# Performance work log

Measured on AMD Instinct MI355X. Metric: run time of the kernel, lower is better.

Reference implementation:

```python
import jax, jax.numpy as jnp
import numpy as np
from jax import lax

H = 512; VS = 32000; VT = 32000; B = 64; TS = 64; TT = 51
PAD = 0


def _lstm_dir(xt, Wih, Whh, bih, bhh):
    # xt: (T, b, h); PyTorch LSTM gate order i,f,g,o
    b = xt.shape[1]
    h0 = jnp.zeros((b, Wih.shape[0] // 4), xt.dtype)
    def step(carry, x):
        h, c = carry
        g = x @ Wih.T + bih + h @ Whh.T + bhh
        i, f, gg, o = jnp.split(g, 4, axis=1)
        c = jax.nn.sigmoid(f) * c + jax.nn.sigmoid(i) * jnp.tanh(gg)
        h = jax.nn.sigmoid(o) * jnp.tanh(c)
        return (h, c), h
    (hT, cT), hs = lax.scan(step, (h0, h0), xt)
    return hs, hT, cT


def _forward(source, target, emb_src, emb_tgt, enc_Wih_f, enc_Whh_f, enc_bih_f, enc_bhh_f,
             enc_Wih_b, enc_Whh_b, enc_bih_b, enc_bhh_b, Wh_w, Wh_b,
             dec_Wih, dec_Whh, dec_bih, dec_bhh, Ws_w, Ws_b, v_w, v_b,
             lin_w, lin_b, out_w, out_b):
    b, ts = source.shape
    h = emb_src.shape[1]
    es = emb_src.at[PAD].set(0.0)  # padding_idx=0 (also zeroes its grad)
    et = emb_tgt.at[PAD].set(0.0)
    # ---- Encoder: bidirectional LSTM, directions summed (all lengths equal) ----
    x = es[source]                       # (b, ts, h); dropout skipped (eval)
    xt = jnp.swapaxes(x, 0, 1)           # (ts, b, h)
    hs_f, hT_f, cT_f = _lstm_dir(xt, enc_Wih_f, enc_Whh_f, enc_bih_f, enc_bhh_f)
    hs_b, hT_b, cT_b = _lstm_dir(xt[::-1], enc_Wih_b, enc_Whh_b, enc_bih_b, enc_bhh_b)
    hs_b = hs_b[::-1]
    enc_out = jnp.swapaxes(hs_f + hs_b, 0, 1)   # (b, ts, h)
    hx = hT_f + hT_b                             # (b, h)
    cx = cT_f + cT_b
    enc_feat_bth = (enc_out.reshape(-1, h) @ Wh_w.T + Wh_b).reshape(b, ts, h)
    # Faithful quirk: mask is eq(PAD) (padding positions = 1), and (ts,b)->(b,ts) is a raw reshape
    mask_bT = (source.T == PAD).astype(x.dtype).reshape(b, ts)
    tgt = target.T  # (tt, b)

    def step(carry, inp):
        hx, cx = carry
        wf, wt = inp
        e = et[wf]                                        # (b, h)
        g = e @ dec_Wih.T + dec_bih + hx @ dec_Whh.T + dec_bhh
        i, f, gg, o = jnp.split(g, 4, axis=1)
        cx = jax.nn.sigmoid(f) * cx + jax.nn.sigmoid(i) * jnp.tanh(gg)
        hx = jax.nn.sigmoid(o) * jnp.tanh(cx)
        # Bahdanau attention
        dec_f = hx @ Ws_w.T + Ws_b
        att = jnp.tanh(enc_feat_bth + dec_f[:, None, :])  # (b, ts, h)
        scores = att @ v_w[0] + v_b[0]                    # (b, ts)
        attn = jax.nn.softmax(scores, axis=1) * mask_bT
        # Faithful quirk: torch .view(-1, b, n) on contiguous (b, ts, n) = raw reshape
        a = attn.reshape(ts, b, 1)
        eo = enc_out.reshape(ts, b, h)
        content = jnp.sum(a * eo, axis=0)                 # (b, h)
        hx_new = jnp.tanh(jnp.concatenate([content, hx], axis=1) @ lin_w.T + lin_b)
        logits = hx_new @ out_w.T + out_b                 # (b, VT)
        logp = jax.nn.log_softmax(logits, axis=1)
        ce = -jnp.take_along_axis(logp, wt[:, None], axis=1)[:, 0]
        valid = (wt != PAD).astype(logits.dtype)          # ignore_index=0
        cnt = valid.sum()
        step_loss = jnp.where(cnt > 0, (ce * valid).sum() / jnp.maximum(cnt, 1.0), 0.0)
        return (hx, cx), step_loss

    (_, _), losses = lax.scan(step, (hx, cx), (tgt[:-1], tgt[1:]))
    return losses.sum()


def setup_inputs() -> dict:
    key = jax.random.key(0)
    ks = jax.random.split(key, 30)
    p = lambda i, s: 0.02 * jax.random.normal(ks[i], s, dtype=jnp.float32)
    return {
        "source": jax.random.randint(ks[0], (B, TS), 0, VS),
        "target": jax.random.randint(ks[1], (B, TT), 0, VT),
        "emb_src": p(2, (VS, H)), "emb_tgt": p(3, (VT, H)),
        "enc_Wih_f": p(4, (4 * H, H)), "enc_Whh_f": p(5, (4 * H, H)),
        "enc_bih_f": p(6, (4 * H,)), "enc_bhh_f": p(7, (4 * H,)),
        "enc_Wih_b": p(8, (4 * H, H)), "enc_Whh_b": p(9, (4 * H, H)),
        "enc_bih_b": p(10, (4 * H,)), "enc_bhh_b": p(11, (4 * H,)),
        "Wh_w": p(12, (H, H)), "Wh_b": p(13, (H,)),
        "dec_Wih": p(14, (4 * H, H)), "dec_Whh": p(15, (4 * H, H)),
        "dec_bih": p(16, (4 * H,)), "dec_bhh": p(17, (4 * H,)),
        "Ws_w": p(18, (H, H)), "Ws_b": p(19, (H,)),
        "v_w": p(20, (1, H)), "v_b": p(21, (1,)),
        "lin_w": p(22, (H, 2 * H)), "lin_b": p(23, (H,)),
        "out_w": p(24, (VT, H)), "out_b": p(25, (VT,)),
    }


def reference(source, target, emb_src, emb_tgt, enc_Wih_f, enc_Whh_f, enc_bih_f, enc_bhh_f,
              enc_Wih_b, enc_Whh_b, enc_bih_b, enc_bhh_b, Wh_w, Wh_b,
              dec_Wih, dec_Whh, dec_bih, dec_bhh, Ws_w, Ws_b, v_w, v_b,
              lin_w, lin_b, out_w, out_b):
    return _forward(source, target, emb_src, emb_tgt, enc_Wih_f, enc_Whh_f, enc_bih_f, enc_bhh_f,
                    enc_Wih_b, enc_Whh_b, enc_bih_b, enc_bhh_b, Wh_w, Wh_b,
                    dec_Wih, dec_Whh, dec_bih, dec_bhh, Ws_w, Ws_b, v_w, v_b,
                    lin_w, lin_b, out_w, out_b)
```

## Files before the change

kernel.cpp:

```cpp
#include <hip/hip_runtime.h>


#define DI __device__ __forceinline__

typedef __attribute__((ext_vector_type(8))) short bf16x8;
typedef __attribute__((ext_vector_type(4))) short s16x4;
typedef __attribute__((ext_vector_type(4))) float f32x4;
typedef const __attribute__((address_space(1))) void* gp1_t;
typedef __attribute__((address_space(3))) void* lp3_t;

DI float bf2f(short u) {
    union { float f; unsigned u; } c; c.u = ((unsigned)(unsigned short)u) << 16; return c.f;
}
DI short f2bf(float f) {
    union { float f; unsigned u; } c; c.f = f;
    unsigned r = c.u + 0x7fffu + ((c.u >> 16) & 1u);
    return (short)(r >> 16);
}
DI float sigm(float x) { return 1.f / (1.f + __expf(-x)); }
DI float tanh_(float x) {
    float e = __expf(-2.f * fabsf(x));
    float r = (1.f - e) / (1.f + e);
    return copysignf(r, x);
}

template<int EPI>
__global__ __launch_bounds__(256) void gemm128(
    const short* __restrict__ A, int lda,
    const short* __restrict__ B, int ldb,
    int K,
    const float* __restrict__ bias,
    void* __restrict__ Cout, int ldc,
    float* __restrict__ partial, int pstride)
{
    __shared__ short lA[8192], lB[8192];
    const int tid = threadIdx.x;
    const int lane = tid & 63, wave = tid >> 6;
    const int wr = wave >> 1, wc = wave & 1;
    const int mbase = blockIdx.y * 128, nbase = blockIdx.x * 128;

    const char* ga[4]; const char* gb[4];
    {
        int r = tid >> 3, sl = tid & 7;
#pragma unroll
        for (int R = 0; R < 4; ++R) {
            int row = R * 32 + r;
            int so = (sl ^ (row & 7)) << 4;
            ga[R] = (const char*)(A + (size_t)(mbase + row) * lda) + so;
            gb[R] = (const char*)(B + (size_t)(nbase + row) * ldb) + so;
        }
    }
    const int r7 = lane & 7, gq = lane >> 4;
    int abase[4], bbase[4];
#pragma unroll
    for (int i = 0; i < 4; ++i) {
        abase[i] = (wr * 64 + i * 16 + (lane & 15)) * 128;
        bbase[i] = (wc * 64 + i * 16 + (lane & 15)) * 128;
    }
    int sloff[2];
#pragma unroll
    for (int h = 0; h < 2; ++h) sloff[h] = ((h * 4 + gq) ^ r7) << 4;

    f32x4 acc[4][4];
#pragma unroll
    for (int i = 0; i < 4; ++i)
#pragma unroll
        for (int j = 0; j < 4; ++j) acc[i][j] = (f32x4){0.f, 0.f, 0.f, 0.f};

    for (int kk = 0; kk < K; kk += 64) {
#pragma unroll
        for (int R = 0; R < 4; ++R)
            __builtin_amdgcn_global_load_lds((gp1_t)ga[R],
                (lp3_t)((char*)lA + R * 4096 + tid * 16), 16, 0, 0);
#pragma unroll
        for (int R = 0; R < 4; ++R)
            __builtin_amdgcn_global_load_lds((gp1_t)gb[R],
                (lp3_t)((char*)lB + R * 4096 + tid * 16), 16, 0, 0);
#pragma unroll
        for (int R = 0; R < 4; ++R) { ga[R] += 128; gb[R] += 128; }
        __syncthreads();
#pragma unroll
        for (int h = 0; h < 2; ++h) {
            bf16x8 af[4], bfv[4];
#pragma unroll
            for (int i = 0; i < 4; ++i)
                af[i] = *(const bf16x8*)((const char*)lA + abase[i] + sloff[h]);
#pragma unroll
            for (int j = 0; j < 4; ++j)
                bfv[j] = *(const bf16x8*)((const char*)lB + bbase[j] + sloff[h]);
#pragma unroll
            for (int i = 0; i < 4; ++i)
#pragma unroll
                for (int j = 0; j < 4; ++j)
                    acc[i][j] = __builtin_amdgcn_mfma_f32_16x16x32_bf16(
                        af[i], bfv[j], acc[i][j], 0, 0, 0);
        }
        __syncthreads();
    }

    float bv[4];
#pragma unroll
    for (int j = 0; j < 4; ++j) bv[j] = bias[nbase + wc * 64 + j * 16 + (lane & 15)];

    if constexpr (EPI == 3) {
#pragma unroll
        for (int i = 0; i < 4; ++i)
#pragma unroll
            for (int r = 0; r < 4; ++r) {
                float es = 0.f;
#pragma unroll
                for (int j = 0; j < 4; ++j) es += __expf(acc[i][j][r] + bv[j]);
                es += __shfl_xor(es, 1); es += __shfl_xor(es, 2);
                es += __shfl_xor(es, 4); es += __shfl_xor(es, 8);
                if ((lane & 15) == 0) {
                    int row = mbase + wr * 64 + i * 16 + (lane >> 4) * 4 + r;
                    partial[(size_t)row * pstride + blockIdx.x * 2 + wc] = es;
                }
            }
    } else {
#pragma unroll
        for (int i = 0; i < 4; ++i)
#pragma unroll
            for (int j = 0; j < 4; ++j)
#pragma unroll
                for (int r = 0; r < 4; ++r) {
                    int row = mbase + wr * 64 + i * 16 + (lane >> 4) * 4 + r;
                    int col = nbase + wc * 64 + j * 16 + (lane & 15);
                    float v = acc[i][j][r] + bv[j];
                    if constexpr (EPI == 0)
                        ((float*)Cout)[(size_t)row * ldc + col] = v;
                    else if constexpr (EPI == 1)
                        ((short*)Cout)[(size_t)row * ldc + col] = f2bf(tanh_(v));
                    else
                        ((short*)Cout)[(size_t)row * ldc + col] = f2bf(v);
                }
    }
}

DI void gbar(int* bar, int target)
{
    __syncthreads();
    if (threadIdx.x == 0) {
        __threadfence();
        atomicAdd(bar, 1);
        while (__hip_atomic_load(bar, __ATOMIC_RELAXED, __HIP_MEMORY_SCOPE_AGENT) < target)
            __builtin_amdgcn_s_sleep(2);
        __threadfence();
    }
    __syncthreads();
}

struct EncDir {
    const short* Whh;
    const short* pre;
    short* hslots;
    float* hs;
    float* cfin;
};

__global__ __launch_bounds__(256) void enc_kernel(EncDir F, EncDir Bd, int* bar)
{
    const int isB = (blockIdx.x >= 32) ? 1 : 0;
    const EncDir E = isB ? Bd : F;
    const int nb = blockIdx.x & 31;
    const int tid = threadIdx.x, lane = tid & 63, wave = tid >> 6;
    const int lc = wave * 16 + (lane & 15);
    const int ncol = nb * 64 + lc;

    bf16x8 bq[16];
    {
        const short* bp = E.Whh + (size_t)ncol * 512 + ((lane >> 4) * 8);
#pragma unroll
        for (int ks = 0; ks < 16; ++ks) bq[ks] = *(const bf16x8*)(bp + ks * 32);
    }
    float cr[4] = {0.f, 0.f, 0.f, 0.f};

    __shared__ short hl[32768];
    __shared__ float g[64 * 65];

    const int swave = tid >> 6, ssl = tid & 63;
    const int r7 = lane & 7, gq = lane >> 4;
    const int hb_base = (lane & 15) << 10;

    for (int s = 0; s < 64; ++s) {
        const char* hsrc = (const char*)E.hslots + (size_t)s * 65536;
#pragma unroll
        for (int R = 0; R < 16; ++R) {
            int row = R * 4 + swave;
            __builtin_amdgcn_global_load_lds(
                (gp1_t)(hsrc + row * 1024 + ((ssl ^ (row & 7)) << 4)),
                (lp3_t)((char*)hl + R * 4096 + tid * 16), 16, 0, 0);
        }
        __syncthreads();

        f32x4 acc[4];
#pragma unroll
        for (int i = 0; i < 4; ++i) acc[i] = (f32x4){0.f, 0.f, 0.f, 0.f};
#pragma unroll
        for (int ks = 0; ks < 16; ++ks) {
            const char* hb = (const char*)hl + hb_base + (((ks * 4 + gq) ^ r7) << 4);
#pragma unroll
            for (int mt = 0; mt < 4; ++mt)
                acc[mt] = __builtin_amdgcn_mfma_f32_16x16x32_bf16(
                    *(const bf16x8*)(hb + mt * 16384), bq[ks], acc[mt], 0, 0, 0);
        }
#pragma unroll
        for (int mt = 0; mt < 4; ++mt)
#pragma unroll
            for (int r = 0; r < 4; ++r)
                g[(mt * 16 + gq * 4 + r) * 65 + lc] = acc[mt][r];
        __syncthreads();

        const int tf = isB ? (63 - s) : s;
        const short* prr = E.pre + (size_t)tf * 131072;
        short* hw = E.hslots + (size_t)(s + 1) * 32768;
        float* hsw = E.hs + (size_t)tf * 32768;
#pragma unroll
        for (int it = 0; it < 4; ++it) {
            int item = tid + it * 256, b = item >> 4, jj = item & 15;
            int j = nb * 16 + jj;
            s16x4 pv = *(const s16x4*)(prr + b * 2048 + nb * 64 + jj * 4);
            float gi = g[b * 65 + jj * 4 + 0] + bf2f(pv.x);
            float gf = g[b * 65 + jj * 4 + 1] + bf2f(pv.y);
            float gg = g[b * 65 + jj * 4 + 2] + bf2f(pv.z);
            float go = g[b * 65 + jj * 4 + 3] + bf2f(pv.w);
            float cn = sigm(gf) * cr[it] + sigm(gi) * tanh_(gg);
            float h = sigm(go) * tanh_(cn);
            cr[it] = cn;
            hw[b * 512 + j] = f2bf(h);
            hsw[b * 512 + j] = h;
            if (s == 63) E.cfin[b * 512 + j] = cn;
        }
        gbar(bar, 64 * (s + 1));
    }
}

__global__ __launch_bounds__(256) void dec_kernel(
    const short* __restrict__ Whh, const short* __restrict__ pre,
    short* __restrict__ hslots, const float* __restrict__ c0,
    short* __restrict__ cat, int* __restrict__ bar)
{
    const int nb = blockIdx.x;
    const int tid = threadIdx.x, lane = tid & 63, wave = tid >> 6;
    const int lc = wave * 16 + (lane & 15);
    const int ncol = nb * 64 + lc;

    bf16x8 bq[16];
    {
        const short* bp = Whh + (size_t)ncol * 512 + ((lane >> 4) * 8);
#pragma unroll
        for (int ks = 0; ks < 16; ++ks) bq[ks] = *(const bf16x8*)(bp + ks * 32);
    }
    float cr[4];
#pragma unroll
    for (int it = 0; it < 4; ++it) {
        int item = tid + it * 256, b = item >> 4, jj = item & 15;
        cr[it] = c0[b * 512 + nb * 16 + jj];
    }

    __shared__ short hl[32768];
    __shared__ float g[64 * 65];
    const int swave = tid >> 6, ssl = tid & 63;
    const int r7 = lane & 7, gq = lane >> 4;
    const int hb_base = (lane & 15) << 10;

    for (int t = 0; t < 50; ++t) {
        const char* hsrc = (const char*)hslots + (size_t)t * 65536;
#pragma unroll
        for (int R = 0; R < 16; ++R) {
            int row = R * 4 + swave;
            __builtin_amdgcn_global_load_lds(
                (gp1_t)(hsrc + row * 1024 + ((ssl ^ (row & 7)) << 4)),
                (lp3_t)((char*)hl + R * 4096 + tid * 16), 16, 0, 0);
        }
        __syncthreads();

        f32x4 acc[4];
#pragma unroll
        for (int i = 0; i < 4; ++i) acc[i] = (f32x4){0.f, 0.f, 0.f, 0.f};
#pragma unroll
        for (int ks = 0; ks < 16; ++ks) {
            const char* hb = (const char*)hl + hb_base + (((ks * 4 + gq) ^ r7) << 4);
#pragma unroll
            for (int mt = 0; mt < 4; ++mt)
                acc[mt] = __builtin_amdgcn_mfma_f32_16x16x32_bf16(
                    *(const bf16x8*)(hb + mt * 16384), bq[ks], acc[mt], 0, 0, 0);
        }
#pragma unroll
        for (int mt = 0; mt < 4; ++mt)
#pragma unroll
            for (int r = 0; r < 4; ++r)
                g[(mt * 16 + gq * 4 + r) * 65 + lc] = acc[mt][r];
        __syncthreads();

        const short* prr = pre + (size_t)t * 131072;
        short* hw = hslots + (size_t)(t + 1) * 32768;
        short* cw = cat + (size_t)t * 65536 + 512;
#pragma unroll
        for (int it = 0; it < 4; ++it) {
            int item = tid + it * 256, b = item >> 4, jj = item & 15;
            int j = nb * 16 + jj;
            s16x4 pv = *(const s16x4*)(prr + b * 2048 + nb * 64 + jj * 4);
            float gi = g[b * 65 + jj * 4 + 0] + bf2f(pv.x);
            float gf = g[b * 65 + jj * 4 + 1] + bf2f(pv.y);
            float gg = g[b * 65 + jj * 4 + 2] + bf2f(pv.z);
            float go = g[b * 65 + jj * 4 + 3] + bf2f(pv.w);
            float cn = sigm(gf) * cr[it] + sigm(gi) * tanh_(gg);
            float h = sigm(go) * tanh_(cn);
            cr[it] = cn;
            hw[b * 512 + j] = f2bf(h);
            cw[b * 1024 + j] = f2bf(h);
        }
        gbar(bar, 32 * (t + 1));
    }
}

struct PrepArgs {
    const float *Wih_f, *Whh_f, *Wih_b, *Whh_b, *Wih_d, *Whh_d;
    short *oWih_f, *oWhh_f, *oWih_b, *oWhh_b, *oWih_d, *oWhh_d;
    const float *Ws, *Wh, *lin, *outw;
    short *oWs, *oWh, *olin, *oout;
    const float *emb_src, *emb_tgt;
    const int *source, *target;
    short *A_src, *A_tgt;
    const float *bihf, *bhhf, *bihb, *bhhb, *bihd, *bhhd;
    float *bsumf, *bsumb, *bsumd;
    int *tgtf;
    short *hF0, *hB0;
    float *dout;
    int *bar;
};

__global__ __launch_bounds__(256) void prep_kernel(PrepArgs P)
{
    const long long total = 6291456LL + 262144 + 262144 + 524288 + 16384000
                          + 2097152 + 1638400 + 6144 + 3200 + 65536 + 3;
    for (long long i = (long long)blockIdx.x * 256 + threadIdx.x; i < total;
         i += (long long)gridDim.x * 256) {
        long long t = i;
        if (t < 6291456LL) {
            int seg = (int)(t >> 20); int r = (int)(t & 1048575);
            int n = r >> 9, k = r & 511;
            int orig = (n & 3) * 512 + (n >> 2);
            const float* s; short* d;
            switch (seg) {
                case 0: s = P.Wih_f; d = P.oWih_f; break;
                case 1: s = P.Whh_f; d = P.oWhh_f; break;
                case 2: s = P.Wih_b; d = P.oWih_b; break;
                case 3: s = P.Whh_b; d = P.oWhh_b; break;
                case 4: s = P.Wih_d; d = P.oWih_d; break;
                default: s = P.Whh_d; d = P.oWhh_d; break;
            }
            d[n * 512 + k] = f2bf(s[orig * 512 + k]);
            continue;
        }
        t -= 6291456LL;
        if (t < 262144) { P.oWs[t] = f2bf(P.Ws[t]); continue; } t -= 262144;
        if (t < 262144) { P.oWh[t] = f2bf(P.Wh[t]); continue; } t -= 262144;
        if (t < 524288) { P.olin[t] = f2bf(P.lin[t]); continue; } t -= 524288;
        if (t < 16384000) { P.oout[t] = f2bf(P.outw[t]); continue; } t -= 16384000;
        if (t < 2097152) {
            int r = (int)(t >> 9), k = (int)(t & 511);
            int tt = r >> 6, b = r & 63;
            int tok = P.source[b * 64 + tt];
            P.A_src[t] = tok ? f2bf(P.emb_src[(size_t)tok * 512 + k]) : (short)0;
            continue;
        } t -= 2097152;
        if (t < 1638400) {
            int r = (int)(t >> 9), k = (int)(t & 511);
            int tt = r >> 6, b = r & 63;
            int tok = P.target[b * 51 + tt];
            P.A_tgt[t] = tok ? f2bf(P.emb_tgt[(size_t)tok * 512 + k]) : (short)0;
            continue;
        } t -= 1638400;
        if (t < 6144) {
            int net = (int)(t >> 11); int n = (int)(t & 2047);
            int orig = (n & 3) * 512 + (n >> 2);
            if (net == 0)      P.bsumf[n] = P.bihf[orig] + P.bhhf[orig];
            else if (net == 1) P.bsumb[n] = P.bihb[orig] + P.bhhb[orig];
            else               P.bsumd[n] = P.bihd[orig] + P.bhhd[orig];
            continue;
        } t -= 6144;
        if (t < 3200) {
            int s = (int)t >> 6, b = (int)t & 63;
            P.tgtf[t] = P.target[b * 51 + s + 1];
            continue;
        } t -= 3200;
        if (t < 65536) {
            if (t < 32768) P.hF0[t] = 0; else P.hB0[t - 32768] = 0;
            continue;
        } t -= 65536;
        if (t == 0) P.dout[0] = 0.f;
        else P.bar[t - 1] = 0;
    }
}

__global__ __launch_bounds__(256) void mid_kernel(
    const float* __restrict__ hsF, const float* __restrict__ hsB,
    const float* __restrict__ cFf, const float* __restrict__ cBf,
    float* __restrict__ enc_out, short* __restrict__ enc_out_bf,
    short* __restrict__ hx0, float* __restrict__ cdec0)
{
    const int total = 64 * 64 * 512 + 64 * 512;
    for (int i = blockIdx.x * 256 + threadIdx.x; i < total; i += gridDim.x * 256) {
        if (i < 64 * 64 * 512) {
            int r = i >> 9, d = i & 511;
            int b = r >> 6, tt = r & 63;
            float v = hsF[(size_t)(tt * 64 + b) * 512 + d] + hsB[(size_t)(tt * 64 + b) * 512 + d];
            enc_out[i] = v;
            enc_out_bf[i] = f2bf(v);
        } else {
            int j = i - 64 * 64 * 512;
            int b = j >> 9, d = j & 511;
            float h0 = hsF[(size_t)(63 * 64 + b) * 512 + d] + hsB[(size_t)(0 * 64 + b) * 512 + d];
            hx0[b * 512 + d] = f2bf(h0);
            cdec0[b * 512 + d] = cFf[b * 512 + d] + cBf[b * 512 + d];
        }
    }
}

__global__ __launch_bounds__(256) void attn_scores(
    const float* __restrict__ enc_feat, const float* __restrict__ dec_f,
    const float* __restrict__ v_w, const float* __restrict__ v_b,
    float* __restrict__ scores)
{
    int p = blockIdx.y;
    int tp = blockIdx.x * 64 + p;
    __shared__ float df[512], vw[512];
    for (int i = threadIdx.x; i < 512; i += 256) {
        df[i] = dec_f[(size_t)tp * 512 + i];
        vw[i] = v_w[i];
    }
    __syncthreads();
    int lane = threadIdx.x & 63, wave = threadIdx.x >> 6;
    float vb = v_b[0];
    for (int q = wave; q < 64; q += 4) {
        const float* ef = enc_feat + (size_t)(p * 64 + q) * 512;
        float s = 0.f;
        for (int d = lane; d < 512; d += 64)
            s += tanh_(ef[d] + df[d]) * vw[d];
        for (int o = 32; o > 0; o >>= 1) s += __shfl_xor(s, o);
        if (lane == 0) scores[(size_t)tp * 64 + q] = s + vb;
    }
}

__global__ __launch_bounds__(256) void softmax_mask(
    float* __restrict__ attn, const int* __restrict__ source)
{
    int row = blockIdx.x * 4 + (threadIdx.x >> 6);
    int lane = threadIdx.x & 63;
    int p = row & 63;
    float v = attn[(size_t)row * 64 + lane];
    float m = v;
    for (int o = 32; o > 0; o >>= 1) m = fmaxf(m, __shfl_xor(m, o));
    float e = __expf(v - m);
    float s = e;
    for (int o = 32; o > 0; o >>= 1) s += __shfl_xor(s, o);
    float mask = (source[lane * 64 + p] == 0) ? 1.f : 0.f;
    attn[(size_t)row * 64 + lane] = (e / s) * mask;
}

__global__ __launch_bounds__(256) void content_cat(
    const float* __restrict__ attn, const float* __restrict__ enc_out,
    short* __restrict__ cat)
{
    int q = blockIdx.y;
    int tq = blockIdx.x * 64 + q;
    __shared__ float ac[64];
    if (threadIdx.x < 64)
        ac[threadIdx.x] = attn[(size_t)(blockIdx.x * 64 + threadIdx.x) * 64 + q];
    __syncthreads();
    for (int d = threadIdx.x; d < 512; d += 256) {
        float s = 0.f;
#pragma unroll 8
        for (int pp = 0; pp < 64; ++pp)
            s += ac[pp] * enc_out[(size_t)(pp * 64 + q) * 512 + d];
        cat[(size_t)tq * 1024 + d] = f2bf(s);
    }
}

__global__ __launch_bounds__(256) void loss_kernel(
    const float* __restrict__ partial, const short* __restrict__ hxnew,
    const short* __restrict__ outw, const float* __restrict__ outb,
    const int* __restrict__ tgtf, float* __restrict__ out)
{
    int t = blockIdx.x;
    int tid = threadIdx.x;
    int b = tid >> 2, c = tid & 3;
    int row = t * 64 + b;
    float s = 0.f;
    for (int j = c; j < 500; j += 4) s += partial[(size_t)row * 500 + j];
    int w = tgtf[row];
    const short* hp = hxnew + (size_t)row * 512 + c * 128;
    const short* wp = outw + (size_t)w * 512 + c * 128;
    float tl = 0.f;
    for (int k2 = 0; k2 < 128; k2 += 8) {
        bf16x8 hv = *(const bf16x8*)(hp + k2);
        bf16x8 wv = *(const bf16x8*)(wp + k2);
#pragma unroll
        for (int u = 0; u < 8; ++u) tl += bf2f(hv[u]) * bf2f(wv[u]);
    }
    s += __shfl_xor(s, 1); s += __shfl_xor(s, 2);
    tl += __shfl_xor(tl, 1); tl += __shfl_xor(tl, 2);
    __shared__ float ce_s[64], va_s[64];
    if (c == 0) {
        float lse = logf(s);
        float ce = lse - (tl + outb[w]);
        float valid = (w != 0) ? 1.f : 0.f;
        ce_s[b] = ce * valid;
        va_s[b] = valid;
    }
    __syncthreads();
    if (tid < 64) {
        float cv = ce_s[tid], vv = va_s[tid];
        for (int o = 32; o > 0; o >>= 1) { cv += __shfl_xor(cv, o); vv += __shfl_xor(vv, o); }
        if (tid == 0) {
            float sl = (vv > 0.f) ? cv / fmaxf(vv, 1.f) : 0.f;
            atomicAdd(out, sl);
        }
    }
}

extern "C" void kernel_launch(void* const* d_in, const int* in_sizes, int n_in,
                              void* d_out, int out_size, void* d_ws, size_t ws_size,
                              hipStream_t stream)
{
    (void)in_sizes; (void)n_in; (void)out_size; (void)ws_size;
    const int*   source  = (const int*)  d_in[0];
    const int*   target  = (const int*)  d_in[1];
    const float* emb_src = (const float*)d_in[2];
    const float* emb_tgt = (const float*)d_in[3];
    const float* eWihF   = (const float*)d_in[4];
    const float* eWhhF   = (const float*)d_in[5];
    const float* ebihF   = (const float*)d_in[6];
    const float* ebhhF   = (const float*)d_in[7];
    const float* eWihB   = (const float*)d_in[8];
    const float* eWhhB   = (const float*)d_in[9];
    const float* ebihB   = (const float*)d_in[10];
    const float* ebhhB   = (const float*)d_in[11];
    const float* Wh_w    = (const float*)d_in[12];
    const float* Wh_b    = (const float*)d_in[13];
    const float* dWih    = (const float*)d_in[14];
    const float* dWhh    = (const float*)d_in[15];
    const float* dbih    = (const float*)d_in[16];
    const float* dbhh    = (const float*)d_in[17];
    const float* Ws_w    = (const float*)d_in[18];
    const float* Ws_b    = (const float*)d_in[19];
    const float* v_w     = (const float*)d_in[20];
    const float* v_b     = (const float*)d_in[21];
    const float* lin_w   = (const float*)d_in[22];
    const float* lin_b   = (const float*)d_in[23];
    const float* out_w   = (const float*)d_in[24];
    const float* out_b   = (const float*)d_in[25];

    char* base = (char*)d_ws;
    size_t off = 0;
    auto alloc = [&](size_t bytes) -> char* {
        char* p = base + off;
        off = (off + bytes + 255) & ~(size_t)255;
        return p;
    };
    short* WihF_bf = (short*)alloc(1048576ULL * 2);
    short* WhhF_bf = (short*)alloc(1048576ULL * 2);
    short* WihB_bf = (short*)alloc(1048576ULL * 2);
    short* WhhB_bf = (short*)alloc(1048576ULL * 2);
    short* WihD_bf = (short*)alloc(1048576ULL * 2);
    short* WhhD_bf = (short*)alloc(1048576ULL * 2);
    short* Ws_bf   = (short*)alloc(262144ULL * 2);
    short* Wh_bf   = (short*)alloc(262144ULL * 2);
    short* lin_bf  = (short*)alloc(524288ULL * 2);
    short* out_bf  = (short*)alloc(16384000ULL * 2);
    short* A_src   = (short*)alloc(2097152ULL * 2);
    short* A_tgt   = (short*)alloc(1638400ULL * 2);
    short* preF    = (short*)alloc(8388608ULL * 2);
    short* preB    = (short*)alloc(8388608ULL * 2);
    short* preD    = (short*)alloc(6553600ULL * 2);
    short* hF_sl   = (short*)alloc(65ULL * 32768 * 2);
    short* hB_sl   = (short*)alloc(65ULL * 32768 * 2);
    short* hxbuf   = (short*)alloc(51ULL * 32768 * 2);
    short* encout_bf = (short*)alloc(2097152ULL * 2);
    short* cat_bf  = (short*)alloc(3276800ULL * 2);
    short* hxnew   = (short*)alloc(1638400ULL * 2);
    float* bsumF   = (float*)alloc(2048 * 4);
    float* bsumB   = (float*)alloc(2048 * 4);
    float* bsumD   = (float*)alloc(2048 * 4);
    float* cFf     = (float*)alloc(32768ULL * 4);
    float* cBf     = (float*)alloc(32768ULL * 4);
    float* cdec0   = (float*)alloc(32768ULL * 4);
    float* hsF     = (float*)alloc(2097152ULL * 4);
    float* hsB     = (float*)alloc(2097152ULL * 4);
    float* enc_out = (float*)alloc(2097152ULL * 4);
    float* enc_feat= (float*)alloc(2097152ULL * 4);
    float* decf    = (float*)alloc(1638400ULL * 4);
    float* attn    = (float*)alloc(204800ULL * 4);
    int*   tgtf    = (int*)  alloc(3200 * 4);
    int*   bar     = (int*)  alloc(16);
    float* partial = (float*)preF;
    float* outp    = (float*)d_out;

    PrepArgs P;
    P.Wih_f = eWihF; P.Whh_f = eWhhF; P.Wih_b = eWihB; P.Whh_b = eWhhB;
    P.Wih_d = dWih;  P.Whh_d = dWhh;
    P.oWih_f = WihF_bf; P.oWhh_f = WhhF_bf; P.oWih_b = WihB_bf; P.oWhh_b = WhhB_bf;
    P.oWih_d = WihD_bf; P.oWhh_d = WhhD_bf;
    P.Ws = Ws_w; P.Wh = Wh_w; P.lin = lin_w; P.outw = out_w;
    P.oWs = Ws_bf; P.oWh = Wh_bf; P.olin = lin_bf; P.oout = out_bf;
    P.emb_src = emb_src; P.emb_tgt = emb_tgt; P.source = source; P.target = target;
    P.A_src = A_src; P.A_tgt = A_tgt;
    P.bihf = ebihF; P.bhhf = ebhhF; P.bihb = ebihB; P.bhhb = ebhhB;
    P.bihd = dbih;  P.bhhd = dbhh;
    P.bsumf = bsumF; P.bsumb = bsumB; P.bsumd = bsumD;
    P.tgtf = tgtf;
    P.hF0 = hF_sl; P.hB0 = hB_sl;
    P.dout = outp; P.bar = bar;
    prep_kernel<<<dim3(2048), 256, 0, stream>>>(P);

    gemm128<4><<<dim3(16, 32), 256, 0, stream>>>(A_src, 512, WihF_bf, 512, 512,
        bsumF, preF, 2048, nullptr, 0);
    gemm128<4><<<dim3(16, 32), 256, 0, stream>>>(A_src, 512, WihB_bf, 512, 512,
        bsumB, preB, 2048, nullptr, 0);
    gemm128<4><<<dim3(16, 25), 256, 0, stream>>>(A_tgt, 512, WihD_bf, 512, 512,
        bsumD, preD, 2048, nullptr, 0);

    EncDir F, Bd;
    F.Whh = WhhF_bf; F.pre = preF; F.hslots = hF_sl; F.hs = hsF; F.cfin = cFf;
    Bd.Whh = WhhB_bf; Bd.pre = preB; Bd.hslots = hB_sl; Bd.hs = hsB; Bd.cfin = cBf;
    enc_kernel<<<dim3(64), 256, 0, stream>>>(F, Bd, bar);

    mid_kernel<<<dim3(1024), 256, 0, stream>>>(hsF, hsB, cFf, cBf,
        enc_out, encout_bf, hxbuf, cdec0);

    gemm128<0><<<dim3(4, 32), 256, 0, stream>>>(encout_bf, 512, Wh_bf, 512, 512,
        Wh_b, enc_feat, 512, nullptr, 0);

    dec_kernel<<<dim3(32), 256, 0, stream>>>(WhhD_bf, preD, hxbuf, cdec0,
        cat_bf, bar + 1);

    gemm128<0><<<dim3(4, 25), 256, 0, stream>>>(hxbuf + 32768, 512, Ws_bf, 512, 512,
        Ws_b, decf, 512, nullptr, 0);
    attn_scores<<<dim3(50, 64), 256, 0, stream>>>(enc_feat, decf, v_w, v_b, attn);
    softmax_mask<<<dim3(800), 256, 0, stream>>>(attn, source);
    content_cat<<<dim3(50, 64), 256, 0, stream>>>(attn, enc_out, cat_bf);
    gemm128<1><<<dim3(4, 25), 256, 0, stream>>>(cat_bf, 1024, lin_bf, 1024, 1024,
        lin_b, hxnew, 512, nullptr, 0);
    gemm128<3><<<dim3(250, 25), 256, 0, stream>>>(hxnew, 512, out_bf, 512, 512,
        out_b, nullptr, 0, partial, 500);
    loss_kernel<<<dim3(50), 256, 0, stream>>>(partial, hxnew, out_bf, out_b,
        tgtf, outp);
}
```

Before: 1.528 ms.

## Lighten persistent LSTM grid barriers with coherent loads and per-direction counters

Drops the thread fences from the grid barrier and replaces them with a vmcnt wait. Hidden-state stores become agent-scope relaxed atomic stores, and loads become agent-scope atomic loads staged through registers into LDS, so cross-block visibility does not depend on cache flushes. The encoder's two directions now sync on separate counters of 32 blocks each, and the last step skips its barrier. It also removes the fp32 hs writes, so mid_kernel rebuilds encoder outputs from the bf16 h slots, which lowers the precision of enc_out. The gate epilogue handles two columns per thread with packed 8-wide loads. The risks are losing the global_load_lds direct path and relying on relaxed ordering being correct.

```diff
diff --git a/kernel.cpp b/kernel.cpp
--- a/kernel.cpp
+++ b/kernel.cpp
@@ -4,7 +4,6 @@
 #define DI __device__ __forceinline__
 
 typedef __attribute__((ext_vector_type(8))) short bf16x8;
-typedef __attribute__((ext_vector_type(4))) short s16x4;
 typedef __attribute__((ext_vector_type(4))) float f32x4;
 typedef const __attribute__((address_space(1))) void* gp1_t;
 typedef __attribute__((address_space(3))) void* lp3_t;
@@ -137,24 +136,47 @@
     }
 }
 
-DI void gbar(int* bar, int target)
-{
+DI void gbarf(int* bar, int target)
+{
+    asm volatile("s_waitcnt vmcnt(0)" ::: "memory");
     __syncthreads();
     if (threadIdx.x == 0) {
-        __threadfence();
         atomicAdd(bar, 1);
         while (__hip_atomic_load(bar, __ATOMIC_RELAXED, __HIP_MEMORY_SCOPE_AGENT) < target)
             __builtin_amdgcn_s_sleep(2);
-        __threadfence();
     }
     __syncthreads();
+}
+
+DI void store_h2(short* p, float h0, float h1)
+{
+    unsigned v = ((unsigned)(unsigned short)f2bf(h0)) |
+                 (((unsigned)(unsigned short)f2bf(h1)) << 16);
+    __hip_atomic_store((unsigned*)p, v, __ATOMIC_RELAXED, __HIP_MEMORY_SCOPE_AGENT);
+}
+
+DI void stage_h_coherent(const char* hsrc, char* hl, int tid, int swave, int ssl)
+{
+    unsigned long long tv[32];
+#pragma unroll
+    for (int R = 0; R < 16; ++R) {
+        int row = R * 4 + swave;
+        const unsigned long long* sp = (const unsigned long long*)
+            (hsrc + row * 1024 + ((ssl ^ (row & 7)) << 4));
+        tv[2 * R]     = __hip_atomic_load(sp,     __ATOMIC_RELAXED, __HIP_MEMORY_SCOPE_AGENT);
+        tv[2 * R + 1] = __hip_atomic_load(sp + 1, __ATOMIC_RELAXED, __HIP_MEMORY_SCOPE_AGENT);
+    }
+#pragma unroll
+    for (int R = 0; R < 16; ++R) {
+        *(unsigned long long*)(hl + R * 4096 + tid * 16)     = tv[2 * R];
+        *(unsigned long long*)(hl + R * 4096 + tid * 16 + 8) = tv[2 * R + 1];
+    }
 }
 
 struct EncDir {
     const short* Whh;
     const short* pre;
     short* hslots;
-    float* hs;
     float* cfin;
 };
 
@@ -162,6 +184,7 @@
 {
     const int isB = (blockIdx.x >= 32) ? 1 : 0;
     const EncDir E = isB ? Bd : F;
+    int* mybar = bar + isB;
     const int nb = blockIdx.x & 31;
     const int tid = threadIdx.x, lane = tid & 63, wave = tid >> 6;
     const int lc = wave * 16 + (lane & 15);
@@ -183,14 +206,8 @@
     const int hb_base = (lane & 15) << 10;
 
     for (int s = 0; s < 64; ++s) {
-        const char* hsrc = (const char*)E.hslots + (size_t)s * 65536;
-#pragma unroll
-        for (int R = 0; R < 16; ++R) {
-            int row = R * 4 + swave;
-            __builtin_amdgcn_global_load_lds(
-                (gp1_t)(hsrc + row * 1024 + ((ssl ^ (row & 7)) << 4)),
-                (lp3_t)((char*)hl + R * 4096 + tid * 16), 16, 0, 0);
-        }
+        stage_h_coherent((const char*)E.hslots + (size_t)s * 65536,
+                         (char*)hl, tid, swave, ssl);
         __syncthreads();
 
         f32x4 acc[4];
@@ -214,24 +231,32 @@
         const int tf = isB ? (63 - s) : s;
         const short* prr = E.pre + (size_t)tf * 131072;
         short* hw = E.hslots + (size_t)(s + 1) * 32768;
-        float* hsw = E.hs + (size_t)tf * 32768;
-#pragma unroll
-        for (int it = 0; it < 4; ++it) {
-            int item = tid + it * 256, b = item >> 4, jj = item & 15;
+#pragma unroll
+        for (int it = 0; it < 2; ++it) {
+            int b = (tid >> 3) + 32 * it;
+            int jj = 2 * (tid & 7);
             int j = nb * 16 + jj;
-            s16x4 pv = *(const s16x4*)(prr + b * 2048 + nb * 64 + jj * 4);
-            float gi = g[b * 65 + jj * 4 + 0] + bf2f(pv.x);
-            float gf = g[b * 65 + jj * 4 + 1] + bf2f(pv.y);
-            float gg = g[b * 65 + jj * 4 + 2] + bf2f(pv.z);
-            float go = g[b * 65 + jj * 4 + 3] + bf2f(pv.w);
-            float cn = sigm(gf) * cr[it] + sigm(gi) * tanh_(gg);
-            float h = sigm(go) * tanh_(cn);
-            cr[it] = cn;
-            hw[b * 512 + j] = f2bf(h);
-            hsw[b * 512 + j] = h;
-            if (s == 63) E.cfin[b * 512 + j] = cn;
-        }
-        gbar(bar, 64 * (s + 1));
+            bf16x8 pv = *(const bf16x8*)(prr + b * 2048 + nb * 64 + jj * 4);
+            float gi0 = g[b * 65 + jj * 4 + 0] + bf2f(pv[0]);
+            float gf0 = g[b * 65 + jj * 4 + 1] + bf2f(pv[1]);
+            float gg0 = g[b * 65 + jj * 4 + 2] + bf2f(pv[2]);
+            float go0 = g[b * 65 + jj * 4 + 3] + bf2f(pv[3]);
+            float gi1 = g[b * 65 + jj * 4 + 4] + bf2f(pv[4]);
+            float gf1 = g[b * 65 + jj * 4 + 5] + bf2f(pv[5]);
+            float gg1 = g[b * 65 + jj * 4 + 6] + bf2f(pv[6]);
+            float go1 = g[b * 65 + jj * 4 + 7] + bf2f(pv[7]);
+            float cn0 = sigm(gf0) * cr[it * 2 + 0] + sigm(gi0) * tanh_(gg0);
+            float cn1 = sigm(gf1) * cr[it * 2 + 1] + sigm(gi1) * tanh_(gg1);
+            float h0 = sigm(go0) * tanh_(cn0);
+            float h1 = sigm(go1) * tanh_(cn1);
+            cr[it * 2 + 0] = cn0; cr[it * 2 + 1] = cn1;
+            store_h2(hw + b * 512 + j, h0, h1);
+            if (s == 63) {
+                E.cfin[b * 512 + j] = cn0;
+                E.cfin[b * 512 + j + 1] = cn1;
+            }
+        }
+        if (s < 63) gbarf(mybar, 32 * (s + 1));
     }
 }
 
@@ -253,9 +278,11 @@
     }
     float cr[4];
 #pragma unroll
-    for (int it = 0; it < 4; ++it) {
-        int item = tid + it * 256, b = item >> 4, jj = item & 15;
-        cr[it] = c0[b * 512 + nb * 16 + jj];
+    for (int it = 0; it < 2; ++it) {
+        int b = (tid >> 3) + 32 * it;
+        int j = nb * 16 + 2 * (tid & 7);
+        cr[it * 2 + 0] = c0[b * 512 + j];
+        cr[it * 2 + 1] = c0[b * 512 + j + 1];
     }
 
     __shared__ short hl[32768];
@@ -265,14 +292,8 @@
     const int hb_base = (lane & 15) << 10;
 
     for (int t = 0; t < 50; ++t) {
-        const char* hsrc = (const char*)hslots + (size_t)t * 65536;
-#pragma unroll
-        for (int R = 0; R < 16; ++R) {
-            int row = R * 4 + swave;
-            __builtin_amdgcn_global_load_lds(
-                (gp1_t)(hsrc + row * 1024 + ((ssl ^ (row & 7)) << 4)),
-                (lp3_t)((char*)hl + R * 4096 + tid * 16), 16, 0, 0);
-        }
+        stage_h_coherent((const char*)hslots + (size_t)t * 65536,
+                         (char*)hl, tid, swave, ssl);
         __syncthreads();
 
         f32x4 acc[4];
@@ -297,21 +318,30 @@
         short* hw = hslots + (size_t)(t + 1) * 32768;
         short* cw = cat + (size_t)t * 65536 + 512;
 #pragma unroll
-        for (int it = 0; it < 4; ++it) {
-            int item = tid + it * 256, b = item >> 4, jj = item & 15;
+        for (int it = 0; it < 2; ++it) {
+            int b = (tid >> 3) + 32 * it;
+            int jj = 2 * (tid & 7);
             int j = nb * 16 + jj;
-            s16x4 pv = *(const s16x4*)(prr + b * 2048 + nb * 64 + jj * 4);
-            float gi = g[b * 65 + jj * 4 + 0] + bf2f(pv.x);
-            float gf = g[b * 65 + jj * 4 + 1] + bf2f(pv.y);
-            float gg = g[b * 65 + jj * 4 + 2] + bf2f(pv.z);
-            float go = g[b * 65 + jj * 4 + 3] + bf2f(pv.w);
-            float cn = sigm(gf) * cr[it] + sigm(gi) * tanh_(gg);
-            float h = sigm(go) * tanh_(cn);
-            cr[it] = cn;
-            hw[b * 512 + j] = f2bf(h);
-            cw[b * 1024 + j] = f2bf(h);
-        }
-        gbar(bar, 32 * (t + 1));
+            bf16x8 pv = *(const bf16x8*)(prr + b * 2048 + nb * 64 + jj * 4);
+            float gi0 = g[b * 65 + jj * 4 + 0] + bf2f(pv[0]);
+            float gf0 = g[b * 65 + jj * 4 + 1] + bf2f(pv[1]);
+            float gg0 = g[b * 65 + jj * 4 + 2] + bf2f(pv[2]);
+            float go0 = g[b * 65 + jj * 4 + 3] + bf2f(pv[3]);
+            float gi1 = g[b * 65 + jj * 4 + 4] + bf2f(pv[4]);
+            float gf1 = g[b * 65 + jj * 4 + 5] + bf2f(pv[5]);
+            float gg1 = g[b * 65 + jj * 4 + 6] + bf2f(pv[6]);
+            float go1 = g[b * 65 + jj * 4 + 7] + bf2f(pv[7]);
+            float cn0 = sigm(gf0) * cr[it * 2 + 0] + sigm(gi0) * tanh_(gg0);
+            float cn1 = sigm(gf1) * cr[it * 2 + 1] + sigm(gi1) * tanh_(gg1);
+            float h0 = sigm(go0) * tanh_(cn0);
+            float h1 = sigm(go1) * tanh_(cn1);
+            cr[it * 2 + 0] = cn0; cr[it * 2 + 1] = cn1;
+            store_h2(hw + b * 512 + j, h0, h1);
+            unsigned cv = ((unsigned)(unsigned short)f2bf(h0)) |
+                          (((unsigned)(unsigned short)f2bf(h1)) << 16);
+            *(unsigned*)(cw + b * 1024 + j) = cv;
+        }
+        if (t < 49) gbarf(bar, 32 * (t + 1));
     }
 }
 
@@ -334,7 +364,7 @@
 __global__ __launch_bounds__(256) void prep_kernel(PrepArgs P)
 {
     const long long total = 6291456LL + 262144 + 262144 + 524288 + 16384000
-                          + 2097152 + 1638400 + 6144 + 3200 + 65536 + 3;
+                          + 2097152 + 1638400 + 6144 + 3200 + 65536 + 5;
     for (long long i = (long long)blockIdx.x * 256 + threadIdx.x; i < total;
          i += (long long)gridDim.x * 256) {
         long long t = i;
@@ -396,7 +426,7 @@
 }
 
 __global__ __launch_bounds__(256) void mid_kernel(
-    const float* __restrict__ hsF, const float* __restrict__ hsB,
+    const short* __restrict__ hFsl, const short* __restrict__ hBsl,
     const float* __restrict__ cFf, const float* __restrict__ cBf,
     float* __restrict__ enc_out, short* __restrict__ enc_out_bf,
     short* __restrict__ hx0, float* __restrict__ cdec0)
@@ -406,13 +436,15 @@
         if (i < 64 * 64 * 512) {
             int r = i >> 9, d = i & 511;
             int b = r >> 6, tt = r & 63;
-            float v = hsF[(size_t)(tt * 64 + b) * 512 + d] + hsB[(size_t)(tt * 64 + b) * 512 + d];
+            float v = bf2f(hFsl[(size_t)(tt + 1) * 32768 + b * 512 + d])
+                    + bf2f(hBsl[(size_t)(64 - tt) * 32768 + b * 512 + d]);
             enc_out[i] = v;
             enc_out_bf[i] = f2bf(v);
         } else {
             int j = i - 64 * 64 * 512;
             int b = j >> 9, d = j & 511;
-            float h0 = hsF[(size_t)(63 * 64 + b) * 512 + d] + hsB[(size_t)(0 * 64 + b) * 512 + d];
+            float h0 = bf2f(hFsl[(size_t)64 * 32768 + b * 512 + d])
+                     + bf2f(hBsl[(size_t)64 * 32768 + b * 512 + d]);
             hx0[b * 512 + d] = f2bf(h0);
             cdec0[b * 512 + d] = cFf[b * 512 + d] + cBf[b * 512 + d];
         }
@@ -587,8 +619,6 @@
     float* cFf     = (float*)alloc(32768ULL * 4);
     float* cBf     = (float*)alloc(32768ULL * 4);
     float* cdec0   = (float*)alloc(32768ULL * 4);
-    float* hsF     = (float*)alloc(2097152ULL * 4);
-    float* hsB     = (float*)alloc(2097152ULL * 4);
     float* enc_out = (float*)alloc(2097152ULL * 4);
     float* enc_feat= (float*)alloc(2097152ULL * 4);
     float* decf    = (float*)alloc(1638400ULL * 4);
@@ -623,18 +653,18 @@
         bsumD, preD, 2048, nullptr, 0);
 
     EncDir F, Bd;
-    F.Whh = WhhF_bf; F.pre = preF; F.hslots = hF_sl; F.hs = hsF; F.cfin = cFf;
-    Bd.Whh = WhhB_bf; Bd.pre = preB; Bd.hslots = hB_sl; Bd.hs = hsB; Bd.cfin = cBf;
+    F.Whh = WhhF_bf; F.pre = preF; F.hslots = hF_sl; F.cfin = cFf;
+    Bd.Whh = WhhB_bf; Bd.pre = preB; Bd.hslots = hB_sl; Bd.cfin = cBf;
     enc_kernel<<<dim3(64), 256, 0, stream>>>(F, Bd, bar);
 
-    mid_kernel<<<dim3(1024), 256, 0, stream>>>(hsF, hsB, cFf, cBf,
+    mid_kernel<<<dim3(1024), 256, 0, stream>>>(hF_sl, hB_sl, cFf, cBf,
         enc_out, encout_bf, hxbuf, cdec0);
 
     gemm128<0><<<dim3(4, 32), 256, 0, stream>>>(encout_bf, 512, Wh_bf, 512, 512,
         Wh_b, enc_feat, 512, nullptr, 0);
 
     dec_kernel<<<dim3(32), 256, 0, stream>>>(WhhD_bf, preD, hxbuf, cdec0,
-        cat_bf, bar + 1);
+        cat_bf, bar + 2);
 
     gemm128<0><<<dim3(4, 25), 256, 0, stream>>>(hxbuf + 32768, 512, Ws_bf, 512, 512,
         Ws_b, decf, 512, nullptr, 0);
```

After: 1.357 ms. 1.13x faster.
